# Kernel optimization log

Hardware: AMD Instinct MI355X
Metric: run time of the kernel (lower is better)

The kernel has to match this reference:

```python
import jax, jax.numpy as jnp
import numpy as np

N = 100_000          # ent_num
D = 256              # ent_dim
E_RAND = 3_200_000   # random edges (avg degree 32); + N self loops
NEG_SLOPE = 0.2      # LeakyReLU slope used by SpGraphAttentionLayer


def setup_inputs() -> dict:
    key = jax.random.key(0)
    k0, k1, k2, k3, k4, k5 = jax.random.split(key, 6)
    edges_rand = jax.random.randint(k0, (2, E_RAND), 0, N, dtype=jnp.int32)
    self_loops = jnp.tile(jnp.arange(N, dtype=jnp.int32)[None, :], (2, 1))
    edges = jnp.concatenate([edges_rand, self_loops], axis=1)  # [2, E]
    scale_w = 1.0 / np.sqrt(D).astype(np.float32)
    scale_a = 0.1 / np.sqrt(D).astype(np.float32)
    emb = jax.random.normal(k1, (N, D), jnp.float32)
    W1 = jax.random.normal(k2, (D, D), jnp.float32) * scale_w
    a1 = jax.random.normal(k3, (2 * D,), jnp.float32) * scale_a
    W2 = jax.random.normal(k4, (D, D), jnp.float32) * scale_w
    a2 = jax.random.normal(k5, (2 * D,), jnp.float32) * scale_a
    return {"emb": emb, "W1": W1, "a1": a1, "W2": W2, "a2": a2, "edges": edges}


def gat_layer(h, W, a, src, dst):
    # h: [N, D] node features; edges (src -> aggregates from dst)
    h2 = h @ W                              # [N, D]
    s_src = h2 @ a[:D]                      # [N] contribution of a . h_src
    s_dst = h2 @ a[D:]                      # [N] contribution of a . h_dst
    score = s_src[src] + s_dst[dst]         # [E] = a . [h_src; h_dst]
    e = jnp.exp(-jax.nn.leaky_relu(score, NEG_SLOPE))  # [E], pyGAT sparse form
    denom = jax.ops.segment_sum(e, src, num_segments=h.shape[0])          # [N]
    num = jax.ops.segment_sum(e[:, None] * h2[dst], src,
                              num_segments=h.shape[0])                    # [N, D]
    return jax.nn.elu(num / denom[:, None])


def reference(emb, W1, a1, W2, a2, edges):
    src, dst = edges[0], edges[1]
    h = gat_layer(emb, W1, a1, src, dst)
    h = gat_layer(h, W2, a2, src, dst)
    return h
```

## Files before the change

### kernel.cpp

```cpp
#include <hip/hip_runtime.h>
#include <hip/hip_bf16.h>

#define D 256
#define NEG_SLOPE 0.2f
#define BM 128
#define BN 128
#define BK 64
#define LDK 72
#define SCAN_CHUNK 1024

using bf16x8 = __attribute__((ext_vector_type(8))) __bf16;
using f32x4  = __attribute__((ext_vector_type(4))) float;
using u32x4  = __attribute__((ext_vector_type(4))) unsigned int;

__device__ __forceinline__ float bf2f(unsigned short u) {
    return __uint_as_float(((unsigned int)u) << 16);
}
__device__ __forceinline__ unsigned short f2bf(float f) {
    unsigned int u = __float_as_uint(f);
    unsigned int r = (u + 0x7FFF + ((u >> 16) & 1)) >> 16;
    return (unsigned short)r;
}


__global__ __launch_bounds__(256) void prep_kernel(
    const float* __restrict__ W1, const float* __restrict__ W2,
    unsigned short* __restrict__ WT1, unsigned short* __restrict__ WT2,
    int4* __restrict__ zbase, int nz16)
{
    const int b = blockIdx.x, tid = threadIdx.x;
    if (b < 256) {
        WT1[(size_t)tid * D + b] = f2bf(W1[(size_t)b * D + tid]);
    } else if (b < 512) {
        const int k = b - 256;
        WT2[(size_t)tid * D + k] = f2bf(W2[(size_t)k * D + tid]);
    } else {
        const int w = (b - 512) * 256 + tid;
        if (w < nz16) zbase[w] = make_int4(0, 0, 0, 0);
    }
}


__global__ void count_kernel(const int* __restrict__ src, int* __restrict__ counts, int E) {
    const int stride = gridDim.x * blockDim.x;
    for (int t = blockIdx.x * blockDim.x + threadIdx.x; t < E; t += stride)
        atomicAdd(&counts[src[t]], 1);
}

__global__ __launch_bounds__(256) void scan_partial_kernel(
    const int* __restrict__ counts, int* __restrict__ partial, int n)
{
    __shared__ int ws[4];
    const int tid = threadIdx.x;
    const int lane = tid & 63, wv = tid >> 6;
    const int idx = blockIdx.x * SCAN_CHUNK + tid * 4;
    int4 v = make_int4(0, 0, 0, 0);
    if (idx + 3 < n) v = *(const int4*)(counts + idx);
    else {
        if (idx + 0 < n) v.x = counts[idx + 0];
        if (idx + 1 < n) v.y = counts[idx + 1];
        if (idx + 2 < n) v.z = counts[idx + 2];
        if (idx + 3 < n) v.w = counts[idx + 3];
    }
    int s = v.x + v.y + v.z + v.w;
    #pragma unroll
    for (int off = 32; off > 0; off >>= 1) s += __shfl_xor(s, off);
    if (lane == 0) ws[wv] = s;
    __syncthreads();
    if (tid == 0) partial[blockIdx.x] = ws[0] + ws[1] + ws[2] + ws[3];
}

__global__ __launch_bounds__(128) void scan_chunks_kernel(
    const int* __restrict__ partial, int* __restrict__ chunkoff,
    int* __restrict__ row_ptr, int nchunks, int n)
{
    __shared__ int sm[128];
    const int tid = threadIdx.x;
    const int v = (tid < nchunks) ? partial[tid] : 0;
    sm[tid] = v;
    __syncthreads();
    #pragma unroll
    for (int off = 1; off < 128; off <<= 1) {
        int t = (tid >= off) ? sm[tid - off] : 0;
        __syncthreads();
        sm[tid] += t;
        __syncthreads();
    }
    if (tid < nchunks) chunkoff[tid] = sm[tid] - v;
    if (tid == 127) row_ptr[n] = sm[127];
}

__global__ __launch_bounds__(256) void scan_write_kernel(
    const int* __restrict__ counts, const int* __restrict__ chunkoff,
    int* __restrict__ row_ptr, int n)
{
    __shared__ int wsum[4];
    const int tid = threadIdx.x;
    const int lane = tid & 63, wv = tid >> 6;
    const int idx = blockIdx.x * SCAN_CHUNK + tid * 4;
    int4 v = make_int4(0, 0, 0, 0);
    if (idx + 3 < n) v = *(const int4*)(counts + idx);
    else {
        if (idx + 0 < n) v.x = counts[idx + 0];
        if (idx + 1 < n) v.y = counts[idx + 1];
        if (idx + 2 < n) v.z = counts[idx + 2];
        if (idx + 3 < n) v.w = counts[idx + 3];
    }
    const int s = v.x + v.y + v.z + v.w;
    int x = s;
    #pragma unroll
    for (int off = 1; off < 64; off <<= 1) {
        int t = __shfl_up(x, off);
        if (lane >= off) x += t;
    }
    if (lane == 63) wsum[wv] = x;
    __syncthreads();
    int wo = chunkoff[blockIdx.x];
    for (int w = 0; w < 4; ++w) if (w < wv) wo += wsum[w];
    int excl = wo + x - s;
    if (idx + 0 < n) row_ptr[idx + 0] = excl;
    if (idx + 1 < n) row_ptr[idx + 1] = excl + v.x;
    if (idx + 2 < n) row_ptr[idx + 2] = excl + v.x + v.y;
    if (idx + 3 < n) row_ptr[idx + 3] = excl + v.x + v.y + v.z;
}

__global__ void fill_kernel(const int* __restrict__ src, const int* __restrict__ dst,
                            const int* __restrict__ row_ptr, int* __restrict__ fillp,
                            int* __restrict__ col, int E) {
    const int stride = gridDim.x * blockDim.x;
    for (int t = blockIdx.x * blockDim.x + threadIdx.x; t < E; t += stride) {
        int s = src[t];
        int pos = atomicAdd(&fillp[s], 1);
        col[row_ptr[s] + pos] = dst[t];
    }
}


__global__ __launch_bounds__(256) void gemm_mfma(
    const unsigned short* __restrict__ Ab, const float* __restrict__ Af,
    const unsigned short* __restrict__ BT,
    unsigned short* __restrict__ C, int M,
    const float* __restrict__ av, float* __restrict__ s_src, float* __restrict__ s_dst)
{
    __shared__ unsigned short smem[2 * BM * LDK];
    unsigned short* As_ = smem;
    unsigned short* Bs_ = smem + BM * LDK;
    const int tid = threadIdx.x;
    const int m0 = blockIdx.x * BM;
    const int n0 = blockIdx.y * BN;
    const int lane = tid & 63;
    const int wv = tid >> 6;
    const int wm = (wv & 1) * 64;
    const int wn = (wv >> 1) * 64;
    const int l15 = lane & 15;
    const int quad = lane >> 4;

    f32x4 acc[4][4];
    #pragma unroll
    for (int i = 0; i < 4; ++i)
        #pragma unroll
        for (int j = 0; j < 4; ++j)
            acc[i][j] = (f32x4){0.f, 0.f, 0.f, 0.f};

    for (int k0 = 0; k0 < D; k0 += BK) {
        #pragma unroll
        for (int c = tid; c < BM * 8; c += 256) {
            const int row = c >> 3, j = c & 7;
            const int gr = m0 + row;
            uint4 avv = make_uint4(0, 0, 0, 0);
            if (gr < M) {
                if (Af) {
                    const float* p = Af + (size_t)gr * D + k0 + j * 8;
                    const float4 f0 = *(const float4*)p;
                    const float4 f1 = *(const float4*)(p + 4);
                    avv.x = (unsigned int)f2bf(f0.x) | ((unsigned int)f2bf(f0.y) << 16);
                    avv.y = (unsigned int)f2bf(f0.z) | ((unsigned int)f2bf(f0.w) << 16);
                    avv.z = (unsigned int)f2bf(f1.x) | ((unsigned int)f2bf(f1.y) << 16);
                    avv.w = (unsigned int)f2bf(f1.z) | ((unsigned int)f2bf(f1.w) << 16);
                } else {
                    avv = *(const uint4*)(Ab + (size_t)gr * D + k0 + j * 8);
                }
            }
            *(uint4*)(As_ + row * LDK + j * 8) = avv;
            const uint4 bv = *(const uint4*)(BT + (size_t)(n0 + row) * D + k0 + j * 8);
            *(uint4*)(Bs_ + row * LDK + j * 8) = bv;
        }
        __syncthreads();
        #pragma unroll
        for (int s = 0; s < 2; ++s) {
            bf16x8 af[4], bfr[4];
            #pragma unroll
            for (int i = 0; i < 4; ++i)
                af[i] = *(const bf16x8*)(As_ + (wm + i * 16 + l15) * LDK + s * 32 + quad * 8);
            #pragma unroll
            for (int j = 0; j < 4; ++j)
                bfr[j] = *(const bf16x8*)(Bs_ + (wn + j * 16 + l15) * LDK + s * 32 + quad * 8);
            #pragma unroll
            for (int i = 0; i < 4; ++i)
                #pragma unroll
                for (int j = 0; j < 4; ++j)
                    acc[i][j] = __builtin_amdgcn_mfma_f32_16x16x32_bf16(
                        af[i], bfr[j], acc[i][j], 0, 0, 0);
        }
        __syncthreads();
    }

    unsigned short* Cw = smem + wv * (64 * LDK);
    #pragma unroll
    for (int i = 0; i < 4; ++i)
        #pragma unroll
        for (int j = 0; j < 4; ++j)
            #pragma unroll
            for (int r = 0; r < 4; ++r)
                Cw[(i * 16 + quad * 4 + r) * LDK + j * 16 + l15] = f2bf(acc[i][j][r]);
    __syncthreads();
    const int ccol = n0 + wn + (lane & 31) * 2;
    const float a1c0 = av[ccol],     a1c1 = av[ccol + 1];
    const float a2c0 = av[D + ccol], a2c1 = av[D + ccol + 1];
    #pragma unroll
    for (int rr = 0; rr < 64; rr += 2) {
        const int row = rr + (lane >> 5);
        const unsigned int wd = *(const unsigned int*)(Cw + row * LDK + (lane & 31) * 2);
        const int gr = m0 + wm + row;
        if (gr < M)
            *(unsigned int*)(C + (size_t)gr * D + ccol) = wd;
        const float f0 = bf2f((unsigned short)(wd & 0xffffu));
        const float f1 = bf2f((unsigned short)(wd >> 16));
        float p1 = f0 * a1c0 + f1 * a1c1;
        float p2 = f0 * a2c0 + f1 * a2c1;
        #pragma unroll
        for (int off = 16; off > 0; off >>= 1) {
            p1 += __shfl_xor(p1, off);
            p2 += __shfl_xor(p2, off);
        }
        if ((lane & 31) == 0 && gr < M) {
            atomicAdd(&s_src[gr], p1);
            atomicAdd(&s_dst[gr], p2);
        }
    }
}


__global__ __launch_bounds__(256) void agg_kernel(
    const unsigned short* __restrict__ h2, const float* __restrict__ s_src,
    const float* __restrict__ s_dst, const int* __restrict__ row_ptr,
    const int* __restrict__ col, unsigned short* __restrict__ out_bf16,
    float* __restrict__ out_f32, int Nn)
{
    const int lane = threadIdx.x & 63;
    const int half = lane >> 5;
    const int hl = lane & 31;
    const int wid = blockIdx.x * 4 + (threadIdx.x >> 6);
    const int nwaves = gridDim.x * 4;
    const unsigned short* hp = h2 + hl * 8;

    for (int node = wid; node < Nn; node += nwaves) {
        const int beg = row_ptr[node], end = row_ptr[node + 1];
        const float ssrc = s_src[node];

        float a[8];
        #pragma unroll
        for (int i = 0; i < 8; ++i) a[i] = 0.f;
        float dpart = 0.f;

        for (int c0 = beg; c0 < end; c0 += 64) {
            const int cnt = min(64, end - c0);
            int j = 0;
            float e = 0.f;
            if (lane < cnt) {
                j = col[c0 + lane];
                const float sc = ssrc + s_dst[j];
                const float l = sc >= 0.f ? sc : NEG_SLOPE * sc;
                e = __expf(-l);
            }
            dpart += e;
            for (int k = 0; k < cnt; k += 8) {
                const int   j0 = __shfl(j, k + 0 + half);
                const int   j1 = __shfl(j, k + 2 + half);
                const int   j2 = __shfl(j, k + 4 + half);
                const int   j3 = __shfl(j, k + 6 + half);
                const float e0 = __shfl(e, k + 0 + half);
                const float e1 = __shfl(e, k + 2 + half);
                const float e2 = __shfl(e, k + 4 + half);
                const float e3 = __shfl(e, k + 6 + half);
                const uint4 u0 = *(const uint4*)(hp + (size_t)j0 * D);
                const uint4 u1 = *(const uint4*)(hp + (size_t)j1 * D);
                const uint4 u2 = *(const uint4*)(hp + (size_t)j2 * D);
                const uint4 u3 = *(const uint4*)(hp + (size_t)j3 * D);
                #define ACC8(u, ev)                                               \
                    a[0] = fmaf(ev, __uint_as_float((u).x << 16), a[0]);          \
                    a[1] = fmaf(ev, __uint_as_float((u).x & 0xffff0000u), a[1]);  \
                    a[2] = fmaf(ev, __uint_as_float((u).y << 16), a[2]);          \
                    a[3] = fmaf(ev, __uint_as_float((u).y & 0xffff0000u), a[3]);  \
                    a[4] = fmaf(ev, __uint_as_float((u).z << 16), a[4]);          \
                    a[5] = fmaf(ev, __uint_as_float((u).z & 0xffff0000u), a[5]);  \
                    a[6] = fmaf(ev, __uint_as_float((u).w << 16), a[6]);          \
                    a[7] = fmaf(ev, __uint_as_float((u).w & 0xffff0000u), a[7]);
                ACC8(u0, e0)
                ACC8(u1, e1)
                ACC8(u2, e2)
                ACC8(u3, e3)
                #undef ACC8
            }
        }

        #pragma unroll
        for (int i = 0; i < 8; ++i) a[i] += __shfl_xor(a[i], 32);

        float denom = dpart;
        #pragma unroll
        for (int off = 32; off > 0; off >>= 1) denom += __shfl_xor(denom, off);
        const float inv = 1.f / denom;

        if (half == 0) {
            float v[8];
            #pragma unroll
            for (int i = 0; i < 8; ++i) {
                const float x = a[i] * inv;
                v[i] = x > 0.f ? x : expm1f(x);
            }
            if (out_bf16) {
                u32x4 o;
                o.x = (unsigned int)f2bf(v[0]) | ((unsigned int)f2bf(v[1]) << 16);
                o.y = (unsigned int)f2bf(v[2]) | ((unsigned int)f2bf(v[3]) << 16);
                o.z = (unsigned int)f2bf(v[4]) | ((unsigned int)f2bf(v[5]) << 16);
                o.w = (unsigned int)f2bf(v[6]) | ((unsigned int)f2bf(v[7]) << 16);
                __builtin_nontemporal_store(o, (u32x4*)(out_bf16 + (size_t)node * D + hl * 8));
            } else {
                float* p = out_f32 + (size_t)node * D + hl * 8;
                f32x4 o0 = {v[0], v[1], v[2], v[3]};
                f32x4 o1 = {v[4], v[5], v[6], v[7]};
                __builtin_nontemporal_store(o0, (f32x4*)p);
                __builtin_nontemporal_store(o1, (f32x4*)(p + 4));
            }
        }
    }
}


static inline size_t align_up(size_t x, size_t a) { return (x + a - 1) & ~(a - 1); }

extern "C" void kernel_launch(void* const* d_in, const int* in_sizes, int n_in,
                              void* d_out, int out_size, void* d_ws, size_t ws_size,
                              hipStream_t stream)
{
    const float* emb = (const float*)d_in[0];
    const float* W1  = (const float*)d_in[1];
    const float* a1  = (const float*)d_in[2];
    const float* W2  = (const float*)d_in[3];
    const float* a2  = (const float*)d_in[4];
    const int* edges = (const int*)d_in[5];
    const int Nn = in_sizes[0] / D;
    const int E  = in_sizes[5] / 2;
    const int* src = edges;
    const int* dst = edges + E;
    const int nchunks = (Nn + SCAN_CHUNK - 1) / SCAN_CHUNK;

    size_t off = 0;
    char* base = (char*)d_ws;
    unsigned short* hA = (unsigned short*)(base + off);
    off = align_up(off + (size_t)Nn * D * sizeof(unsigned short), 256);
    unsigned short* hB = (unsigned short*)(base + off);
    off = align_up(off + (size_t)Nn * D * sizeof(unsigned short), 256);
    unsigned short* WT1 = (unsigned short*)(base + off);
    off = align_up(off + (size_t)D * D * sizeof(unsigned short), 256);
    unsigned short* WT2 = (unsigned short*)(base + off);
    off = align_up(off + (size_t)D * D * sizeof(unsigned short), 256);

    const size_t cstride = align_up((size_t)Nn * sizeof(int), 256);
    char* zstart = base + off;
    float* s1s = (float*)(base + off); off += (size_t)Nn * sizeof(float);
    float* s1d = (float*)(base + off); off += (size_t)Nn * sizeof(float);
    float* s2s = (float*)(base + off); off += (size_t)Nn * sizeof(float);
    float* s2d = (float*)(base + off); off += (size_t)Nn * sizeof(float);
    off = align_up(off, 256);
    int* counts  = (int*)(base + off);   off += cstride;
    int* fillp   = (int*)(base + off);   off += cstride;
    const size_t zbytes = (size_t)(base + off - zstart);
    const int nz16 = (int)(zbytes / 16);

    int* row_ptr = (int*)(base + off);   off = align_up(off + (size_t)(Nn + 1) * sizeof(int), 256);
    int* partial = (int*)(base + off);   off = align_up(off + (size_t)nchunks * sizeof(int), 256);
    int* chunkoff= (int*)(base + off);   off = align_up(off + (size_t)nchunks * sizeof(int), 256);
    int* col     = (int*)(base + off);   off = align_up(off + (size_t)E * sizeof(int), 256);

    const int zblocks = (nz16 + 255) / 256;
    prep_kernel<<<512 + zblocks, 256, 0, stream>>>(W1, W2, WT1, WT2, (int4*)zstart, nz16);

    count_kernel<<<2048, 256, 0, stream>>>(src, counts, E);
    scan_partial_kernel<<<nchunks, 256, 0, stream>>>(counts, partial, Nn);
    scan_chunks_kernel<<<1, 128, 0, stream>>>(partial, chunkoff, row_ptr, nchunks, Nn);
    scan_write_kernel<<<nchunks, 256, 0, stream>>>(counts, chunkoff, row_ptr, Nn);
    fill_kernel<<<2048, 256, 0, stream>>>(src, dst, row_ptr, fillp, col, E);

    dim3 ggrid((Nn + BM - 1) / BM, D / BN);
    gemm_mfma<<<ggrid, 256, 0, stream>>>(nullptr, emb, WT1, hA, Nn, a1, s1s, s1d);
    agg_kernel<<<2048, 256, 0, stream>>>(hA, s1s, s1d, row_ptr, col, hB, nullptr, Nn);
    gemm_mfma<<<ggrid, 256, 0, stream>>>(hB, nullptr, WT2, hA, Nn, a2, s2s, s2d);
    agg_kernel<<<2048, 256, 0, stream>>>(hA, s2s, s2d, row_ptr, col, nullptr,
                                         (float*)d_out, Nn);
}
```

Measured before the change: 1.089 ms.

## Split aggregation into two feature-half passes with one node per wave

```diff
diff --git a/kernel.cpp b/kernel.cpp
--- a/kernel.cpp
+++ b/kernel.cpp
@@ -42,9 +42,8 @@
 
 
 __global__ void count_kernel(const int* __restrict__ src, int* __restrict__ counts, int E) {
-    const int stride = gridDim.x * blockDim.x;
-    for (int t = blockIdx.x * blockDim.x + threadIdx.x; t < E; t += stride)
-        atomicAdd(&counts[src[t]], 1);
+    int t = blockIdx.x * blockDim.x + threadIdx.x;
+    if (t < E) atomicAdd(&counts[src[t]], 1);
 }
 
 __global__ __launch_bounds__(256) void scan_partial_kernel(
@@ -127,8 +126,8 @@
 __global__ void fill_kernel(const int* __restrict__ src, const int* __restrict__ dst,
                             const int* __restrict__ row_ptr, int* __restrict__ fillp,
                             int* __restrict__ col, int E) {
-    const int stride = gridDim.x * blockDim.x;
-    for (int t = blockIdx.x * blockDim.x + threadIdx.x; t < E; t += stride) {
+    int t = blockIdx.x * blockDim.x + threadIdx.x;
+    if (t < E) {
         int s = src[t];
         int pos = atomicAdd(&fillp[s], 1);
         col[row_ptr[s] + pos] = dst[t];
@@ -245,94 +244,95 @@
     const unsigned short* __restrict__ h2, const float* __restrict__ s_src,
     const float* __restrict__ s_dst, const int* __restrict__ row_ptr,
     const int* __restrict__ col, unsigned short* __restrict__ out_bf16,
-    float* __restrict__ out_f32, int Nn)
+    float* __restrict__ out_f32, int Nn, int dhalf)
 {
     const int lane = threadIdx.x & 63;
-    const int half = lane >> 5;
-    const int hl = lane & 31;
-    const int wid = blockIdx.x * 4 + (threadIdx.x >> 6);
-    const int nwaves = gridDim.x * 4;
-    const unsigned short* hp = h2 + hl * 8;
-
-    for (int node = wid; node < Nn; node += nwaves) {
-        const int beg = row_ptr[node], end = row_ptr[node + 1];
-        const float ssrc = s_src[node];
-
-        float a[8];
-        #pragma unroll
-        for (int i = 0; i < 8; ++i) a[i] = 0.f;
-        float dpart = 0.f;
-
-        for (int c0 = beg; c0 < end; c0 += 64) {
-            const int cnt = min(64, end - c0);
-            int j = 0;
-            float e = 0.f;
-            if (lane < cnt) {
-                j = col[c0 + lane];
-                const float sc = ssrc + s_dst[j];
-                const float l = sc >= 0.f ? sc : NEG_SLOPE * sc;
-                e = __expf(-l);
-            }
-            dpart += e;
-            for (int k = 0; k < cnt; k += 8) {
-                const int   j0 = __shfl(j, k + 0 + half);
-                const int   j1 = __shfl(j, k + 2 + half);
-                const int   j2 = __shfl(j, k + 4 + half);
-                const int   j3 = __shfl(j, k + 6 + half);
-                const float e0 = __shfl(e, k + 0 + half);
-                const float e1 = __shfl(e, k + 2 + half);
-                const float e2 = __shfl(e, k + 4 + half);
-                const float e3 = __shfl(e, k + 6 + half);
-                const uint4 u0 = *(const uint4*)(hp + (size_t)j0 * D);
-                const uint4 u1 = *(const uint4*)(hp + (size_t)j1 * D);
-                const uint4 u2 = *(const uint4*)(hp + (size_t)j2 * D);
-                const uint4 u3 = *(const uint4*)(hp + (size_t)j3 * D);
-                #define ACC8(u, ev)                                               \
-                    a[0] = fmaf(ev, __uint_as_float((u).x << 16), a[0]);          \
-                    a[1] = fmaf(ev, __uint_as_float((u).x & 0xffff0000u), a[1]);  \
-                    a[2] = fmaf(ev, __uint_as_float((u).y << 16), a[2]);          \
-                    a[3] = fmaf(ev, __uint_as_float((u).y & 0xffff0000u), a[3]);  \
-                    a[4] = fmaf(ev, __uint_as_float((u).z << 16), a[4]);          \
-                    a[5] = fmaf(ev, __uint_as_float((u).z & 0xffff0000u), a[5]);  \
-                    a[6] = fmaf(ev, __uint_as_float((u).w << 16), a[6]);          \
-                    a[7] = fmaf(ev, __uint_as_float((u).w & 0xffff0000u), a[7]);
-                ACC8(u0, e0)
-                ACC8(u1, e1)
-                ACC8(u2, e2)
-                ACC8(u3, e3)
-                #undef ACC8
-            }
-        }
-
-        #pragma unroll
-        for (int i = 0; i < 8; ++i) a[i] += __shfl_xor(a[i], 32);
-
-        float denom = dpart;
-        #pragma unroll
-        for (int off = 32; off > 0; off >>= 1) denom += __shfl_xor(denom, off);
-        const float inv = 1.f / denom;
-
-        if (half == 0) {
-            float v[8];
-            #pragma unroll
-            for (int i = 0; i < 8; ++i) {
-                const float x = a[i] * inv;
-                v[i] = x > 0.f ? x : expm1f(x);
-            }
-            if (out_bf16) {
-                u32x4 o;
-                o.x = (unsigned int)f2bf(v[0]) | ((unsigned int)f2bf(v[1]) << 16);
-                o.y = (unsigned int)f2bf(v[2]) | ((unsigned int)f2bf(v[3]) << 16);
-                o.z = (unsigned int)f2bf(v[4]) | ((unsigned int)f2bf(v[5]) << 16);
-                o.w = (unsigned int)f2bf(v[6]) | ((unsigned int)f2bf(v[7]) << 16);
-                __builtin_nontemporal_store(o, (u32x4*)(out_bf16 + (size_t)node * D + hl * 8));
-            } else {
-                float* p = out_f32 + (size_t)node * D + hl * 8;
-                f32x4 o0 = {v[0], v[1], v[2], v[3]};
-                f32x4 o1 = {v[4], v[5], v[6], v[7]};
-                __builtin_nontemporal_store(o0, (f32x4*)p);
-                __builtin_nontemporal_store(o1, (f32x4*)(p + 4));
-            }
+    const int q  = lane >> 4;
+    const int ql = lane & 15;
+    const int node = blockIdx.x * 4 + (threadIdx.x >> 6);
+    if (node >= Nn) return;
+    const int beg = row_ptr[node], end = row_ptr[node + 1];
+    const float ssrc = s_src[node];
+    const unsigned short* hp = h2 + dhalf * 128 + ql * 8;
+
+    float a[8];
+    #pragma unroll
+    for (int i = 0; i < 8; ++i) a[i] = 0.f;
+    float dpart = 0.f;
+
+    for (int c0 = beg; c0 < end; c0 += 64) {
+        const int cnt = min(64, end - c0);
+        int j = 0;
+        float e = 0.f;
+        if (lane < cnt) {
+            j = col[c0 + lane];
+            const float sc = ssrc + s_dst[j];
+            const float l = sc >= 0.f ? sc : NEG_SLOPE * sc;
+            e = __expf(-l);
+        }
+        dpart += e;
+        for (int k = 0; k < cnt; k += 16) {
+            const int   j0 = __shfl(j, k + 0  + q);
+            const int   j1 = __shfl(j, k + 4  + q);
+            const int   j2 = __shfl(j, k + 8  + q);
+            const int   j3 = __shfl(j, k + 12 + q);
+            const float e0 = __shfl(e, k + 0  + q);
+            const float e1 = __shfl(e, k + 4  + q);
+            const float e2 = __shfl(e, k + 8  + q);
+            const float e3 = __shfl(e, k + 12 + q);
+            const uint4 u0 = *(const uint4*)(hp + (size_t)j0 * D);
+            const uint4 u1 = *(const uint4*)(hp + (size_t)j1 * D);
+            const uint4 u2 = *(const uint4*)(hp + (size_t)j2 * D);
+            const uint4 u3 = *(const uint4*)(hp + (size_t)j3 * D);
+            #define ACC8(u, ev)                                               \
+                a[0] = fmaf(ev, __uint_as_float((u).x << 16), a[0]);          \
+                a[1] = fmaf(ev, __uint_as_float((u).x & 0xffff0000u), a[1]);  \
+                a[2] = fmaf(ev, __uint_as_float((u).y << 16), a[2]);          \
+                a[3] = fmaf(ev, __uint_as_float((u).y & 0xffff0000u), a[3]);  \
+                a[4] = fmaf(ev, __uint_as_float((u).z << 16), a[4]);          \
+                a[5] = fmaf(ev, __uint_as_float((u).z & 0xffff0000u), a[5]);  \
+                a[6] = fmaf(ev, __uint_as_float((u).w << 16), a[6]);          \
+                a[7] = fmaf(ev, __uint_as_float((u).w & 0xffff0000u), a[7]);
+            ACC8(u0, e0)
+            ACC8(u1, e1)
+            ACC8(u2, e2)
+            ACC8(u3, e3)
+            #undef ACC8
+        }
+    }
+
+    #pragma unroll
+    for (int i = 0; i < 8; ++i) {
+        a[i] += __shfl_xor(a[i], 16);
+        a[i] += __shfl_xor(a[i], 32);
+    }
+
+    float denom = dpart;
+    #pragma unroll
+    for (int off = 32; off > 0; off >>= 1) denom += __shfl_xor(denom, off);
+    const float inv = 1.f / denom;
+
+    if (q == 0) {
+        float v[8];
+        #pragma unroll
+        for (int i = 0; i < 8; ++i) {
+            const float x = a[i] * inv;
+            v[i] = x > 0.f ? x : expm1f(x);
+        }
+        if (out_bf16) {
+            u32x4 o;
+            o.x = (unsigned int)f2bf(v[0]) | ((unsigned int)f2bf(v[1]) << 16);
+            o.y = (unsigned int)f2bf(v[2]) | ((unsigned int)f2bf(v[3]) << 16);
+            o.z = (unsigned int)f2bf(v[4]) | ((unsigned int)f2bf(v[5]) << 16);
+            o.w = (unsigned int)f2bf(v[6]) | ((unsigned int)f2bf(v[7]) << 16);
+            __builtin_nontemporal_store(
+                o, (u32x4*)(out_bf16 + (size_t)node * D + dhalf * 128 + ql * 8));
+        } else {
+            float* p = out_f32 + (size_t)node * D + dhalf * 128 + ql * 8;
+            f32x4 o0 = {v[0], v[1], v[2], v[3]};
+            f32x4 o1 = {v[4], v[5], v[6], v[7]};
+            __builtin_nontemporal_store(o0, (f32x4*)p);
+            __builtin_nontemporal_store(o1, (f32x4*)(p + 4));
         }
     }
 }
@@ -387,16 +387,20 @@
     const int zblocks = (nz16 + 255) / 256;
     prep_kernel<<<512 + zblocks, 256, 0, stream>>>(W1, W2, WT1, WT2, (int4*)zstart, nz16);
 
-    count_kernel<<<2048, 256, 0, stream>>>(src, counts, E);
+    count_kernel<<<(E + 255) / 256, 256, 0, stream>>>(src, counts, E);
     scan_partial_kernel<<<nchunks, 256, 0, stream>>>(counts, partial, Nn);
     scan_chunks_kernel<<<1, 128, 0, stream>>>(partial, chunkoff, row_ptr, nchunks, Nn);
     scan_write_kernel<<<nchunks, 256, 0, stream>>>(counts, chunkoff, row_ptr, Nn);
-    fill_kernel<<<2048, 256, 0, stream>>>(src, dst, row_ptr, fillp, col, E);
+    fill_kernel<<<(E + 255) / 256, 256, 0, stream>>>(src, dst, row_ptr, fillp, col, E);
 
     dim3 ggrid((Nn + BM - 1) / BM, D / BN);
+    const int agrid = (Nn + 3) / 4;
     gemm_mfma<<<ggrid, 256, 0, stream>>>(nullptr, emb, WT1, hA, Nn, a1, s1s, s1d);
-    agg_kernel<<<2048, 256, 0, stream>>>(hA, s1s, s1d, row_ptr, col, hB, nullptr, Nn);
+    agg_kernel<<<agrid, 256, 0, stream>>>(hA, s1s, s1d, row_ptr, col, hB, nullptr, Nn, 0);
+    agg_kernel<<<agrid, 256, 0, stream>>>(hA, s1s, s1d, row_ptr, col, hB, nullptr, Nn, 1);
     gemm_mfma<<<ggrid, 256, 0, stream>>>(hB, nullptr, WT2, hA, Nn, a2, s2s, s2d);
-    agg_kernel<<<2048, 256, 0, stream>>>(hA, s2s, s2d, row_ptr, col, nullptr,
-                                         (float*)d_out, Nn);
-}
+    agg_kernel<<<agrid, 256, 0, stream>>>(hA, s2s, s2d, row_ptr, col, nullptr,
+                                          (float*)d_out, Nn, 0);
+    agg_kernel<<<agrid, 256, 0, stream>>>(hA, s2s, s2d, row_ptr, col, nullptr,
+                                          (float*)d_out, Nn, 1);
+}
```

Measured after the change: 1.031 ms. -5.3%, faster.
